# Kernel optimization log

Measured on AMD Instinct MI355X. Metric: run time of the kernel, lower is better.

Reference implementation:

```python
import jax, jax.numpy as jnp
import numpy as np

BIT_DEPTH = 8  # feature squeezing

def setup_inputs() -> dict:
    key = jax.random.key(0)
    ks = jax.random.split(key, 8)
    B, C, H, W = 8, 256, 64, 64
    Cq = C // 8
    x = jax.random.normal(ks[0], (B, C, H, W), dtype=jnp.float32)
    # 1x1 conv weights stored as [out, in] (kernel dims squeezed)
    wq = jax.random.normal(ks[1], (Cq, C), dtype=jnp.float32) * 0.05
    bq = jax.random.normal(ks[2], (Cq,), dtype=jnp.float32) * 0.05
    wk = jax.random.normal(ks[3], (Cq, C), dtype=jnp.float32) * 0.05
    bk = jax.random.normal(ks[4], (Cq,), dtype=jnp.float32) * 0.05
    wv = jax.random.normal(ks[5], (C, C), dtype=jnp.float32) * 0.05
    bv = jax.random.normal(ks[6], (C,), dtype=jnp.float32) * 0.05
    gamma = jax.random.normal(ks[7], (1,), dtype=jnp.float32) * 0.1
    return {"x": x, "wq": wq, "bq": bq, "wk": wk, "bk": bk, "wv": wv, "bv": bv, "gamma": gamma}

def reference(x, wq, bq, wk, bk, wv, bv, gamma):
    B, C, H, W = x.shape
    N = H * W
    xf = x.reshape(B, C, N)  # flatten spatial
    # 1x1 convs == per-pixel linear projections
    q = jnp.einsum('bcn,oc->bon', xf, wq) + bq[None, :, None]   # [B, C/8, N]
    k = jnp.einsum('bcn,oc->bon', xf, wk) + bk[None, :, None]   # [B, C/8, N]
    v = jnp.einsum('bcn,oc->bon', xf, wv) + bv[None, :, None]   # [B, C, N]
    energy = jnp.einsum('bcn,bcm->bnm', q, k)                   # [B, N, N] (no scaling, as in source)
    attn = jax.nn.softmax(energy, axis=-1)
    out = jnp.einsum('bcm,bnm->bcn', v, attn).reshape(B, C, H, W)
    out = gamma[0] * out + out               # gamma-scaled residual of attention output
    scale = jnp.float32(2 ** BIT_DEPTH)
    return jnp.floor(out * scale) / scale    # feature squeezing (bit_depth=8)
```

## Files before the change

### kernel.cpp

```cpp
#include <hip/hip_runtime.h>
#include <math.h>

namespace {
constexpr int BB = 8;
constexpr int CH = 256;
constexpr int CQ = 32;
constexpr int NN = 4096;
}

typedef float f32x4 __attribute__((ext_vector_type(4)));
typedef short bf16x8 __attribute__((ext_vector_type(8)));
typedef unsigned short us8 __attribute__((ext_vector_type(8)));

#define MFMA16(a, b, c) __builtin_amdgcn_mfma_f32_16x16x32_bf16(a, b, c, 0, 0, 0)
#define LOG2E 1.4426950408889634f

__device__ __forceinline__ unsigned short f2bf(float x) {
    unsigned int u = __float_as_uint(x);
    u += 0x7fffu + ((u >> 16) & 1u);
    return (unsigned short)(u >> 16);
}
__device__ __forceinline__ float bf2f(unsigned short h) {
    return __uint_as_float(((unsigned int)h) << 16);
}
__device__ __forceinline__ void gload16(const void* g, void* l) {
    __builtin_amdgcn_global_load_lds(
        (const __attribute__((address_space(1))) unsigned int*)g,
        (__attribute__((address_space(3))) unsigned int*)l, 16, 0, 0);
}

__global__ __launch_bounds__(256) void wsplit_kernel(
    const float* __restrict__ wq, const float* __restrict__ wk,
    const float* __restrict__ wv,
    unsigned short* __restrict__ wh, unsigned short* __restrict__ wl)
{
    int idx = blockIdx.x * 256 + threadIdx.x;
    float v;
    if (idx < 8192)       v = wq[idx];
    else if (idx < 16384) v = wk[idx - 8192];
    else                  v = wv[idx - 16384];
    unsigned short hi = f2bf(v);
    wh[idx] = hi;
    wl[idx] = f2bf(v - bf2f(hi));
}

#define PJ_XL 32768
#define PJ_VE 16384
__global__ __launch_bounds__(256, 2) void proj_kernel(
    const float* __restrict__ x,
    const unsigned short* __restrict__ wh, const unsigned short* __restrict__ wl,
    const float* __restrict__ bq, const float* __restrict__ bk,
    const float* __restrict__ bv,
    unsigned short* __restrict__ qh, unsigned short* __restrict__ ql,
    unsigned short* __restrict__ kh, unsigned short* __restrict__ kl,
    unsigned short* __restrict__ vt)
{
    __shared__ __align__(16) unsigned char smem[65536];
    const int t    = threadIdx.x;
    const int lane = t & 63;
    const int w    = t >> 6;
    const int l16  = lane & 15;
    const int quad = lane >> 4;
    const int b    = blockIdx.x >> 6;
    const int n0   = (blockIdx.x & 63) << 6;

    const float* xB = x + (size_t)b * 256 * NN + n0;
    const int n = lane;

    {
        int cc = w;
        float v[8];
        #pragma unroll
        for (int j = 0; j < 8; ++j)
            v[j] = xB[(size_t)(cc * 8 + j) * NN + n];
        us8 h8, l8;
        #pragma unroll
        for (int j = 0; j < 8; ++j) {
            unsigned short hi = f2bf(v[j]);
            h8[j] = hi;
            l8[j] = f2bf(v[j] - bf2f(hi));
        }
        int off = n * 512 + ((cc ^ (n & 7)) << 4);
        *(us8*)(smem + off) = h8;
        *(us8*)(smem + PJ_XL + off) = l8;
    }
    __syncthreads();

    f32x4 acc[5][4] = {};
    #pragma unroll 1
    for (int kc = 0; kc < 8; ++kc) {
        float vnext[8];
        if (kc < 7) {
            int cc = (kc + 1) * 4 + w;
            #pragma unroll
            for (int j = 0; j < 8; ++j)
                vnext[j] = xB[(size_t)(cc * 8 + j) * NN + n];
        }

        bf16x8 ah[5], al[5];
        #pragma unroll
        for (int i = 0; i < 5; ++i) {
            int och = (w * 5 + i) * 16 + l16;
            ah[i] = *(const bf16x8*)(wh + och * 256 + kc * 32 + quad * 8);
            al[i] = *(const bf16x8*)(wl + och * 256 + kc * 32 + quad * 8);
        }
        #pragma unroll
        for (int nt = 0; nt < 4; ++nt) {
            int roff = (nt * 16 + l16) * 512 + (((kc * 4 + quad) ^ (l16 & 7)) * 16);
            bf16x8 bh = *(const bf16x8*)(smem + roff);
            bf16x8 bl = *(const bf16x8*)(smem + PJ_XL + roff);
            #pragma unroll
            for (int i = 0; i < 5; ++i) {
                acc[i][nt] = MFMA16(ah[i], bh, acc[i][nt]);
                acc[i][nt] = MFMA16(al[i], bh, acc[i][nt]);
                acc[i][nt] = MFMA16(ah[i], bl, acc[i][nt]);
            }
        }

        if (kc < 7) {
            int cc = (kc + 1) * 4 + w;
            us8 h8, l8;
            #pragma unroll
            for (int j = 0; j < 8; ++j) {
                unsigned short hi = f2bf(vnext[j]);
                h8[j] = hi;
                l8[j] = f2bf(vnext[j] - bf2f(hi));
            }
            int off = n * 512 + ((cc ^ (n & 7)) << 4);
            *(us8*)(smem + off) = h8;
            *(us8*)(smem + PJ_XL + off) = l8;
        }
        __syncthreads();
    }

    #pragma unroll
    for (int i = 0; i < 5; ++i) {
        int tile = w * 5 + i;
        if (tile < 4) {
            #pragma unroll
            for (int r = 0; r < 4; ++r) {
                int och = tile * 16 + quad * 4 + r;
                float bias = (och < 32) ? bq[och] : bk[och - 32];
                int arr = (och < 32) ? 0 : 2;
                int oq = och & 31;
                #pragma unroll
                for (int nt = 0; nt < 4; ++nt) {
                    float val = acc[i][nt][r] + bias;
                    if (och < 32) val *= LOG2E;
                    unsigned short hi = f2bf(val);
                    unsigned short lo = f2bf(val - bf2f(hi));
                    *(unsigned short*)(smem + arr * 4096 + (nt * 16 + l16) * 64 + oq * 2) = hi;
                    *(unsigned short*)(smem + (arr + 1) * 4096 + (nt * 16 + l16) * 64 + oq * 2) = lo;
                }
            }
        } else {
            #pragma unroll
            for (int r = 0; r < 4; ++r) {
                int voch = tile * 16 + quad * 4 + r - 64;
                float bias = bv[voch];
                #pragma unroll
                for (int nt = 0; nt < 4; ++nt) {
                    *(unsigned short*)(smem + PJ_VE + voch * 136 + (nt * 16 + l16) * 2)
                        = f2bf(acc[i][nt][r] + bias);
                }
            }
        }
    }
    __syncthreads();

    {
        unsigned short* dsts[4] = { qh, ql, kh, kl };
        int arr = t >> 6, nn = t & 63;
        unsigned short* dst = dsts[arr] + ((size_t)b * NN + n0 + nn) * 32;
        #pragma unroll
        for (int i = 0; i < 4; ++i)
            *(us8*)(dst + i * 8) = *(const us8*)(smem + arr * 4096 + nn * 64 + i * 16);
    }
    #pragma unroll
    for (int p = 0; p < 4; ++p) {
        int voch = p * 64 + (t >> 2), piece = t & 3;
        unsigned short* dst = vt + ((size_t)b * CH + voch) * NN + n0 + piece * 16;
        *(us8*)(dst)     = *(const us8*)(smem + PJ_VE + voch * 136 + piece * 32);
        *(us8*)(dst + 8) = *(const us8*)(smem + PJ_VE + voch * 136 + piece * 32 + 16);
    }
}

#define A_P0 0
#define A_P1 8192
#define A_V0 16384
#define A_V1 49152
#define A_SM 16384

__global__ __launch_bounds__(256, 2) void attn_kernel(
    const unsigned short* __restrict__ qh, const unsigned short* __restrict__ ql,
    const unsigned short* __restrict__ kh, const unsigned short* __restrict__ kl,
    const unsigned short* __restrict__ vt, const float* __restrict__ gptr,
    float* __restrict__ out)
{
    __shared__ __align__(16) unsigned char smem[81920];
    const int t    = threadIdx.x;
    const int lane = t & 63;
    const int w    = t >> 6;
    const int l16  = lane & 15;
    const int quad = lane >> 4;
    const int b    = blockIdx.x & 7;
    const int n0   = (blockIdx.x >> 3) << 6;

    bf16x8 qhA[4], qlA[4];
    #pragma unroll
    for (int qt = 0; qt < 4; ++qt) {
        size_t row = (size_t)b * NN + n0 + qt * 16 + l16;
        qhA[qt] = *(const bf16x8*)(qh + row * 32 + quad * 8);
        qlA[qt] = *(const bf16x8*)(ql + row * 32 + quad * 8);
    }

    const unsigned short* khbase = kh + ((size_t)b * NN + w * 16 + l16) * 32 + quad * 8;
    const unsigned short* klbase = kl + ((size_t)b * NN + w * 16 + l16) * 32 + quad * 8;
    const unsigned char*  vtB    = (const unsigned char*)(vt + (size_t)b * CH * NN);

    const unsigned char* vsrc[8];
    int vlds[8];
    #pragma unroll
    for (int j = 0; j < 8; ++j) {
        int idx = j * 256 + t;
        int r = idx >> 3, cl = idx & 7;
        int cg = cl ^ (r & 7);
        vsrc[j] = vtB + (size_t)r * 8192 + cg * 16;
        vlds[j] = idx * 16;
    }
    const int poff = l16 * 128 + ((((w << 1) | (quad >> 1)) ^ (l16 & 7)) << 4)
                   + ((quad & 1) << 3);

    f32x4 acc[4][4] = {};
    float S[4] = {};

    bf16x8 kch = *(const bf16x8*)(khbase);
    bf16x8 kcl = *(const bf16x8*)(klbase);
    #pragma unroll
    for (int j = 0; j < 8; ++j)
        gload16(vsrc[j], smem + A_V0 + vlds[j]);

    #pragma unroll 1
    for (int tile = 0; tile < 64; ++tile) {
        unsigned char* P = smem + ((tile & 1) ? A_P1 : A_P0);

        f32x4 e4[4];
        __builtin_amdgcn_s_setprio(1);
        #pragma unroll
        for (int qt = 0; qt < 4; ++qt) {
            f32x4 e = { 0.f, 0.f, 0.f, 0.f };
            e = MFMA16(kch, qhA[qt], e);
            e = MFMA16(kch, qlA[qt], e);
            e = MFMA16(kcl, qhA[qt], e);
            e4[qt] = e;
        }
        __builtin_amdgcn_s_setprio(0);

        #pragma unroll
        for (int qt = 0; qt < 4; ++qt) {
            float p0 = exp2f(e4[qt][0]), p1 = exp2f(e4[qt][1]);
            float p2 = exp2f(e4[qt][2]), p3 = exp2f(e4[qt][3]);
            unsigned int u01, u23;
            asm("v_cvt_pk_bf16_f32 %0, %1, %2" : "=v"(u01) : "v"(p0), "v"(p1));
            asm("v_cvt_pk_bf16_f32 %0, %1, %2" : "=v"(u23) : "v"(p2), "v"(p3));
            S[qt] += (__uint_as_float(u01 << 16) + __uint_as_float(u01 & 0xffff0000u))
                   + (__uint_as_float(u23 << 16) + __uint_as_float(u23 & 0xffff0000u));
            int2 pk2 = { (int)u01, (int)u23 };
            *(int2*)(P + qt * 2048 + poff) = pk2;
        }

        __syncthreads();

        const int m1 = ((tile + 1) & 63) * 64;
        bf16x8 knh = *(const bf16x8*)(khbase + (size_t)m1 * 32);
        bf16x8 knl = *(const bf16x8*)(klbase + (size_t)m1 * 32);
        if (tile < 63) {
            unsigned char* vdst = smem + ((tile & 1) ? A_V0 : A_V1);
            #pragma unroll
            for (int j = 0; j < 8; ++j) {
                vsrc[j] += 128;
                gload16(vsrc[j], vdst + vlds[j]);
            }
        }

        const unsigned char* VB = smem + ((tile & 1) ? A_V1 : A_V0);
        bf16x8 af0[4], af1[4], bf0[4], bf1[4];
        #pragma unroll
        for (int qt = 0; qt < 4; ++qt) {
            int row = qt * 16 + l16;
            af0[qt] = *(const bf16x8*)(P + row * 128
                                         + (((0 * 4 + quad) ^ (l16 & 7)) << 4));
            af1[qt] = *(const bf16x8*)(P + row * 128
                                         + (((1 * 4 + quad) ^ (l16 & 7)) << 4));
        }
        #pragma unroll
        for (int ct = 0; ct < 4; ++ct) {
            int vrow = w * 64 + ct * 16 + l16;
            bf0[ct] = *(const bf16x8*)(VB + vrow * 128
                                          + (((0 * 4 + quad) ^ (l16 & 7)) << 4));
            bf1[ct] = *(const bf16x8*)(VB + vrow * 128
                                          + (((1 * 4 + quad) ^ (l16 & 7)) << 4));
        }
        __builtin_amdgcn_s_setprio(1);
        #pragma unroll
        for (int qt = 0; qt < 4; ++qt)
            #pragma unroll
            for (int ct = 0; ct < 4; ++ct)
                acc[qt][ct] = MFMA16(af0[qt], bf0[ct], acc[qt][ct]);
        #pragma unroll
        for (int qt = 0; qt < 4; ++qt)
            #pragma unroll
            for (int ct = 0; ct < 4; ++ct)
                acc[qt][ct] = MFMA16(af1[qt], bf1[ct], acc[qt][ct]);
        __builtin_amdgcn_s_setprio(0);

        kch = knh;
        kcl = knl;
    }

    #pragma unroll
    for (int mask = 16; mask <= 32; mask <<= 1)
        #pragma unroll
        for (int qt = 0; qt < 4; ++qt)
            S[qt] += __shfl_xor(S[qt], mask);
    float* SM = (float*)(smem + A_SM);
    if (quad == 0) {
        #pragma unroll
        for (int qt = 0; qt < 4; ++qt)
            SM[w * 64 + qt * 16 + l16] = S[qt];
    }
    __syncthreads();

    const float g1 = 1.f + gptr[0];
    float* ob = out + (size_t)b * CH * NN;
    #pragma unroll
    for (int qt = 0; qt < 4; ++qt) {
        float is[4];
        #pragma unroll
        for (int r = 0; r < 4; ++r) {
            int qi = qt * 16 + quad * 4 + r;
            float Sf = SM[qi] + SM[64 + qi] + SM[128 + qi] + SM[192 + qi];
            is[r] = g1 / Sf;
        }
        #pragma unroll
        for (int ct = 0; ct < 4; ++ct) {
            float4 o4;
            o4.x = floorf(acc[qt][ct][0] * is[0] * 256.f) * 0.00390625f;
            o4.y = floorf(acc[qt][ct][1] * is[1] * 256.f) * 0.00390625f;
            o4.z = floorf(acc[qt][ct][2] * is[2] * 256.f) * 0.00390625f;
            o4.w = floorf(acc[qt][ct][3] * is[3] * 256.f) * 0.00390625f;
            *(float4*)(ob + (size_t)(w * 64 + ct * 16 + l16) * NN
                          + n0 + qt * 16 + quad * 4) = o4;
        }
    }
}

extern "C" void kernel_launch(void* const* d_in, const int* in_sizes, int n_in,
                              void* d_out, int out_size, void* d_ws, size_t ws_size,
                              hipStream_t stream) {
    const float* x  = (const float*)d_in[0];
    const float* wq = (const float*)d_in[1];
    const float* bq = (const float*)d_in[2];
    const float* wk = (const float*)d_in[3];
    const float* bk = (const float*)d_in[4];
    const float* wv = (const float*)d_in[5];
    const float* bv = (const float*)d_in[6];
    const float* gm = (const float*)d_in[7];
    float* out = (float*)d_out;

    unsigned short* ws = (unsigned short*)d_ws;
    const size_t WSZ = 320 * 256;
    const size_t QSZ = (size_t)BB * NN * 32;
    const size_t XSZ = (size_t)BB * NN * 256;
    unsigned short* wh = ws;
    unsigned short* wl = wh + WSZ;
    unsigned short* qh = wl + WSZ;
    unsigned short* ql = qh + QSZ;
    unsigned short* kh = ql + QSZ;
    unsigned short* kl = kh + QSZ;
    unsigned short* vt = kl + QSZ;

    wsplit_kernel<<<320, 256, 0, stream>>>(wq, wk, wv, wh, wl);
    proj_kernel<<<512, 256, 0, stream>>>(x, wh, wl, bq, bk, bv,
                                         qh, ql, kh, kl, vt);
    attn_kernel<<<512, 256, 0, stream>>>(qh, ql, kh, kl, vt, gm, out);
}
```

Measured before the change: 223.6 us.

## Halve projection tile width to 32 pixels and double block count

The projection kernel now processes 32 spatial positions per block instead of 64. It launches 1024 blocks, uses 32KB of shared memory, and declares launch bounds for 4 blocks per CU. The load schedule becomes 4 stages of 8 channel groups, and the LDS staging and store mapping for Q/K/V are reworked to fit. The goal is more occupancy and parallelism in the projection stage, at the cost of reloading the weight fragments twice as often per pixel. The attention kernel, which likely dominates total time, is unchanged.

```diff
diff --git a/kernel.cpp b/kernel.cpp
--- a/kernel.cpp
+++ b/kernel.cpp
@@ -44,9 +44,7 @@
     wl[idx] = f2bf(v - bf2f(hi));
 }
 
-#define PJ_XL 32768
-#define PJ_VE 16384
-__global__ __launch_bounds__(256, 2) void proj_kernel(
+__global__ __launch_bounds__(256, 4) void proj_kernel(
     const float* __restrict__ x,
     const unsigned short* __restrict__ wh, const unsigned short* __restrict__ wl,
     const float* __restrict__ bq, const float* __restrict__ bk,
@@ -55,20 +53,21 @@
     unsigned short* __restrict__ kh, unsigned short* __restrict__ kl,
     unsigned short* __restrict__ vt)
 {
-    __shared__ __align__(16) unsigned char smem[65536];
+    __shared__ __align__(16) unsigned char smem[32768];
     const int t    = threadIdx.x;
     const int lane = t & 63;
     const int w    = t >> 6;
     const int l16  = lane & 15;
     const int quad = lane >> 4;
-    const int b    = blockIdx.x >> 6;
-    const int n0   = (blockIdx.x & 63) << 6;
+    const int b    = blockIdx.x >> 7;
+    const int n0   = (blockIdx.x & 127) << 5;
 
     const float* xB = x + (size_t)b * 256 * NN + n0;
-    const int n = lane;
+    const int n   = t & 31;
+    const int cg0 = t >> 5;
 
     {
-        int cc = w;
+        int cc = cg0;
         float v[8];
         #pragma unroll
         for (int j = 0; j < 8; ++j)
@@ -82,43 +81,48 @@
         }
         int off = n * 512 + ((cc ^ (n & 7)) << 4);
         *(us8*)(smem + off) = h8;
-        *(us8*)(smem + PJ_XL + off) = l8;
+        *(us8*)(smem + 16384 + off) = l8;
     }
     __syncthreads();
 
-    f32x4 acc[5][4] = {};
+    f32x4 acc[5][2] = {};
     #pragma unroll 1
-    for (int kc = 0; kc < 8; ++kc) {
+    for (int s = 0; s < 4; ++s) {
         float vnext[8];
-        if (kc < 7) {
-            int cc = (kc + 1) * 4 + w;
+        if (s < 3) {
+            int cc = (s + 1) * 8 + cg0;
             #pragma unroll
             for (int j = 0; j < 8; ++j)
                 vnext[j] = xB[(size_t)(cc * 8 + j) * NN + n];
         }
 
-        bf16x8 ah[5], al[5];
-        #pragma unroll
-        for (int i = 0; i < 5; ++i) {
-            int och = (w * 5 + i) * 16 + l16;
-            ah[i] = *(const bf16x8*)(wh + och * 256 + kc * 32 + quad * 8);
-            al[i] = *(const bf16x8*)(wl + och * 256 + kc * 32 + quad * 8);
-        }
-        #pragma unroll
-        for (int nt = 0; nt < 4; ++nt) {
-            int roff = (nt * 16 + l16) * 512 + (((kc * 4 + quad) ^ (l16 & 7)) * 16);
-            bf16x8 bh = *(const bf16x8*)(smem + roff);
-            bf16x8 bl = *(const bf16x8*)(smem + PJ_XL + roff);
+        #pragma unroll
+        for (int kh2 = 0; kh2 < 2; ++kh2) {
+            int kc = s * 2 + kh2;
+            bf16x8 ah[5], al[5];
             #pragma unroll
             for (int i = 0; i < 5; ++i) {
-                acc[i][nt] = MFMA16(ah[i], bh, acc[i][nt]);
-                acc[i][nt] = MFMA16(al[i], bh, acc[i][nt]);
-                acc[i][nt] = MFMA16(ah[i], bl, acc[i][nt]);
-            }
-        }
-
-        if (kc < 7) {
-            int cc = (kc + 1) * 4 + w;
+                int och = (w * 5 + i) * 16 + l16;
+                ah[i] = *(const bf16x8*)(wh + och * 256 + kc * 32 + quad * 8);
+                al[i] = *(const bf16x8*)(wl + och * 256 + kc * 32 + quad * 8);
+            }
+            #pragma unroll
+            for (int nt = 0; nt < 2; ++nt) {
+                int roff = (nt * 16 + l16) * 512
+                         + (((kc * 4 + quad) ^ (l16 & 7)) * 16);
+                bf16x8 bh = *(const bf16x8*)(smem + roff);
+                bf16x8 bl = *(const bf16x8*)(smem + 16384 + roff);
+                #pragma unroll
+                for (int i = 0; i < 5; ++i) {
+                    acc[i][nt] = MFMA16(ah[i], bh, acc[i][nt]);
+                    acc[i][nt] = MFMA16(al[i], bh, acc[i][nt]);
+                    acc[i][nt] = MFMA16(ah[i], bl, acc[i][nt]);
+                }
+            }
+        }
+
+        if (s < 3) {
+            int cc = (s + 1) * 8 + cg0;
             us8 h8, l8;
             #pragma unroll
             for (int j = 0; j < 8; ++j) {
@@ -128,7 +132,7 @@
             }
             int off = n * 512 + ((cc ^ (n & 7)) << 4);
             *(us8*)(smem + off) = h8;
-            *(us8*)(smem + PJ_XL + off) = l8;
+            *(us8*)(smem + 16384 + off) = l8;
         }
         __syncthreads();
     }
@@ -144,13 +148,13 @@
                 int arr = (och < 32) ? 0 : 2;
                 int oq = och & 31;
                 #pragma unroll
-                for (int nt = 0; nt < 4; ++nt) {
+                for (int nt = 0; nt < 2; ++nt) {
                     float val = acc[i][nt][r] + bias;
                     if (och < 32) val *= LOG2E;
                     unsigned short hi = f2bf(val);
                     unsigned short lo = f2bf(val - bf2f(hi));
-                    *(unsigned short*)(smem + arr * 4096 + (nt * 16 + l16) * 64 + oq * 2) = hi;
-                    *(unsigned short*)(smem + (arr + 1) * 4096 + (nt * 16 + l16) * 64 + oq * 2) = lo;
+                    *(unsigned short*)(smem + arr * 2048 + (nt * 16 + l16) * 64 + oq * 2) = hi;
+                    *(unsigned short*)(smem + (arr + 1) * 2048 + (nt * 16 + l16) * 64 + oq * 2) = lo;
                 }
             }
         } else {
@@ -159,8 +163,8 @@
                 int voch = tile * 16 + quad * 4 + r - 64;
                 float bias = bv[voch];
                 #pragma unroll
-                for (int nt = 0; nt < 4; ++nt) {
-                    *(unsigned short*)(smem + PJ_VE + voch * 136 + (nt * 16 + l16) * 2)
+                for (int nt = 0; nt < 2; ++nt) {
+                    *(unsigned short*)(smem + 8192 + voch * 72 + (nt * 16 + l16) * 2)
                         = f2bf(acc[i][nt][r] + bias);
                 }
             }
@@ -170,18 +174,18 @@
 
     {
         unsigned short* dsts[4] = { qh, ql, kh, kl };
-        int arr = t >> 6, nn = t & 63;
-        unsigned short* dst = dsts[arr] + ((size_t)b * NN + n0 + nn) * 32;
+        int arr = t >> 6, sub = t & 63;
+        int row = sub >> 1, half = sub & 1;
+        unsigned short* dst = dsts[arr] + ((size_t)b * NN + n0 + row) * 32 + half * 16;
+        *(us8*)(dst)     = *(const us8*)(smem + arr * 2048 + row * 64 + half * 32);
+        *(us8*)(dst + 8) = *(const us8*)(smem + arr * 2048 + row * 64 + half * 32 + 8 * 2);
+    }
+    {
+        int voch = t;
+        unsigned short* dst = vt + ((size_t)b * CH + voch) * NN + n0;
         #pragma unroll
         for (int i = 0; i < 4; ++i)
-            *(us8*)(dst + i * 8) = *(const us8*)(smem + arr * 4096 + nn * 64 + i * 16);
-    }
-    #pragma unroll
-    for (int p = 0; p < 4; ++p) {
-        int voch = p * 64 + (t >> 2), piece = t & 3;
-        unsigned short* dst = vt + ((size_t)b * CH + voch) * NN + n0 + piece * 16;
-        *(us8*)(dst)     = *(const us8*)(smem + PJ_VE + voch * 136 + piece * 32);
-        *(us8*)(dst + 8) = *(const us8*)(smem + PJ_VE + voch * 136 + piece * 32 + 16);
+            *(us8*)(dst + i * 8) = *(const us8*)(smem + 8192 + voch * 72 + i * 16);
     }
 }
 
@@ -381,7 +385,7 @@
     unsigned short* vt = kl + QSZ;
 
     wsplit_kernel<<<320, 256, 0, stream>>>(wq, wk, wv, wh, wl);
-    proj_kernel<<<512, 256, 0, stream>>>(x, wh, wl, bq, bk, bv,
-                                         qh, ql, kh, kl, vt);
+    proj_kernel<<<1024, 256, 0, stream>>>(x, wh, wl, bq, bk, bv,
+                                          qh, ql, kh, kl, vt);
     attn_kernel<<<512, 256, 0, stream>>>(qh, ql, kh, kl, vt, gm, out);
 }
```

Measured after the change: 265.6 us. +18.8%, slower.

## Split projection output channels across two blocks with double-buffered small LDS

Applied to the files above, without the earlier changes.

The projection kernel now launches twice as many blocks, each handling half the output-channel tiles (12 or 8 tiles), so per-thread accumulators shrink from 5 to 3 tiles. The staged x slice is reduced to a double-buffered 8 KB chunk per k-step instead of holding all 256 channels, cutting LDS from 64 KB to about 33 KB and allowing four blocks per CU. The trade-off is that each x tile is loaded and bf16-split twice, once per half, and the channel split is uneven across the two halves.

```diff
diff --git a/kernel.cpp b/kernel.cpp
--- a/kernel.cpp
+++ b/kernel.cpp
@@ -44,9 +44,7 @@
     wl[idx] = f2bf(v - bf2f(hi));
 }
 
-#define PJ_XL 32768
-#define PJ_VE 16384
-__global__ __launch_bounds__(256, 2) void proj_kernel(
+__global__ __launch_bounds__(256, 4) void proj_kernel(
     const float* __restrict__ x,
     const unsigned short* __restrict__ wh, const unsigned short* __restrict__ wl,
     const float* __restrict__ bq, const float* __restrict__ bk,
@@ -55,24 +53,27 @@
     unsigned short* __restrict__ kh, unsigned short* __restrict__ kl,
     unsigned short* __restrict__ vt)
 {
-    __shared__ __align__(16) unsigned char smem[65536];
+    __shared__ __align__(16) unsigned char smem[33792];
     const int t    = threadIdx.x;
     const int lane = t & 63;
     const int w    = t >> 6;
     const int l16  = lane & 15;
     const int quad = lane >> 4;
-    const int b    = blockIdx.x >> 6;
-    const int n0   = (blockIdx.x & 63) << 6;
+    const int b    = blockIdx.x >> 7;
+    const int h    = blockIdx.x & 1;
+    const int n0   = ((blockIdx.x >> 1) & 63) << 6;
+    const int NT   = h ? 2 : 3;
 
     const float* xB = x + (size_t)b * 256 * NN + n0;
     const int n = lane;
+    const int woff = n * 64 + ((w ^ (n & 3) ^ ((n >> 2) & 3)) << 4);
+    const int rsw  = ((l16 & 3) ^ ((l16 >> 2) & 3));
 
     {
-        int cc = w;
         float v[8];
         #pragma unroll
         for (int j = 0; j < 8; ++j)
-            v[j] = xB[(size_t)(cc * 8 + j) * NN + n];
+            v[j] = xB[(size_t)(w * 8 + j) * NN + n];
         us8 h8, l8;
         #pragma unroll
         for (int j = 0; j < 8; ++j) {
@@ -80,45 +81,49 @@
             h8[j] = hi;
             l8[j] = f2bf(v[j] - bf2f(hi));
         }
-        int off = n * 512 + ((cc ^ (n & 7)) << 4);
-        *(us8*)(smem + off) = h8;
-        *(us8*)(smem + PJ_XL + off) = l8;
+        *(us8*)(smem + woff) = h8;
+        *(us8*)(smem + 4096 + woff) = l8;
     }
     __syncthreads();
 
-    f32x4 acc[5][4] = {};
+    f32x4 acc[3][4] = {};
     #pragma unroll 1
     for (int kc = 0; kc < 8; ++kc) {
         float vnext[8];
         if (kc < 7) {
-            int cc = (kc + 1) * 4 + w;
             #pragma unroll
             for (int j = 0; j < 8; ++j)
-                vnext[j] = xB[(size_t)(cc * 8 + j) * NN + n];
-        }
-
-        bf16x8 ah[5], al[5];
-        #pragma unroll
-        for (int i = 0; i < 5; ++i) {
-            int och = (w * 5 + i) * 16 + l16;
-            ah[i] = *(const bf16x8*)(wh + och * 256 + kc * 32 + quad * 8);
-            al[i] = *(const bf16x8*)(wl + och * 256 + kc * 32 + quad * 8);
+                vnext[j] = xB[(size_t)((kc + 1) * 32 + w * 8 + j) * NN + n];
+        }
+
+        const int base = (kc & 1) * 8192;
+        bf16x8 ah[3], al[3];
+        #pragma unroll
+        for (int i = 0; i < 3; ++i) {
+            if (i < NT) {
+                int tile = h ? (12 + w * 2 + i) : (w * 3 + i);
+                int och  = tile * 16 + l16;
+                ah[i] = *(const bf16x8*)(wh + och * 256 + kc * 32 + quad * 8);
+                al[i] = *(const bf16x8*)(wl + och * 256 + kc * 32 + quad * 8);
+            }
         }
         #pragma unroll
         for (int nt = 0; nt < 4; ++nt) {
-            int roff = (nt * 16 + l16) * 512 + (((kc * 4 + quad) ^ (l16 & 7)) * 16);
-            bf16x8 bh = *(const bf16x8*)(smem + roff);
-            bf16x8 bl = *(const bf16x8*)(smem + PJ_XL + roff);
-            #pragma unroll
-            for (int i = 0; i < 5; ++i) {
-                acc[i][nt] = MFMA16(ah[i], bh, acc[i][nt]);
-                acc[i][nt] = MFMA16(al[i], bh, acc[i][nt]);
-                acc[i][nt] = MFMA16(ah[i], bl, acc[i][nt]);
+            int roff = (nt * 16 + l16) * 64 + ((quad ^ rsw) << 4);
+            bf16x8 bh = *(const bf16x8*)(smem + base + roff);
+            bf16x8 bl = *(const bf16x8*)(smem + base + 4096 + roff);
+            #pragma unroll
+            for (int i = 0; i < 3; ++i) {
+                if (i < NT) {
+                    acc[i][nt] = MFMA16(ah[i], bh, acc[i][nt]);
+                    acc[i][nt] = MFMA16(al[i], bh, acc[i][nt]);
+                    acc[i][nt] = MFMA16(ah[i], bl, acc[i][nt]);
+                }
             }
         }
 
         if (kc < 7) {
-            int cc = (kc + 1) * 4 + w;
+            const int nb = ((kc + 1) & 1) * 8192;
             us8 h8, l8;
             #pragma unroll
             for (int j = 0; j < 8; ++j) {
@@ -126,16 +131,16 @@
                 h8[j] = hi;
                 l8[j] = f2bf(vnext[j] - bf2f(hi));
             }
-            int off = n * 512 + ((cc ^ (n & 7)) << 4);
-            *(us8*)(smem + off) = h8;
-            *(us8*)(smem + PJ_XL + off) = l8;
+            *(us8*)(smem + nb + woff) = h8;
+            *(us8*)(smem + nb + 4096 + woff) = l8;
         }
         __syncthreads();
     }
 
     #pragma unroll
-    for (int i = 0; i < 5; ++i) {
-        int tile = w * 5 + i;
+    for (int i = 0; i < 3; ++i) {
+        if (i >= NT) continue;
+        int tile = h ? (12 + w * 2 + i) : (w * 3 + i);
         if (tile < 4) {
             #pragma unroll
             for (int r = 0; r < 4; ++r) {
@@ -156,11 +161,12 @@
         } else {
             #pragma unroll
             for (int r = 0; r < 4; ++r) {
-                int voch = tile * 16 + quad * 4 + r - 64;
-                float bias = bv[voch];
+                int vloc = tile * 16 + quad * 4 + r - (h ? 192 : 64);
+                float bias = bv[vloc + (h ? 128 : 0)];
+                int vb = h ? 0 : 16384;
                 #pragma unroll
                 for (int nt = 0; nt < 4; ++nt) {
-                    *(unsigned short*)(smem + PJ_VE + voch * 136 + (nt * 16 + l16) * 2)
+                    *(unsigned short*)(smem + vb + vloc * 136 + (nt * 16 + l16) * 2)
                         = f2bf(acc[i][nt][r] + bias);
                 }
             }
@@ -168,20 +174,26 @@
     }
     __syncthreads();
 
-    {
+    if (h == 0) {
         unsigned short* dsts[4] = { qh, ql, kh, kl };
-        int arr = t >> 6, nn = t & 63;
-        unsigned short* dst = dsts[arr] + ((size_t)b * NN + n0 + nn) * 32;
+        int arr = t >> 6, nn2 = t & 63;
+        unsigned short* dst = dsts[arr] + ((size_t)b * NN + n0 + nn2) * 32;
         #pragma unroll
         for (int i = 0; i < 4; ++i)
-            *(us8*)(dst + i * 8) = *(const us8*)(smem + arr * 4096 + nn * 64 + i * 16);
-    }
-    #pragma unroll
-    for (int p = 0; p < 4; ++p) {
-        int voch = p * 64 + (t >> 2), piece = t & 3;
-        unsigned short* dst = vt + ((size_t)b * CH + voch) * NN + n0 + piece * 16;
-        *(us8*)(dst)     = *(const us8*)(smem + PJ_VE + voch * 136 + piece * 32);
-        *(us8*)(dst + 8) = *(const us8*)(smem + PJ_VE + voch * 136 + piece * 32 + 16);
+            *(us8*)(dst + i * 8) = *(const us8*)(smem + arr * 4096 + nn2 * 64 + i * 16);
+        int voch = t >> 1, piece = t & 1;
+        unsigned short* vd = vt + ((size_t)b * CH + voch) * NN + n0 + piece * 32;
+        const unsigned char* src = smem + 16384 + voch * 136 + piece * 64;
+        #pragma unroll
+        for (int i = 0; i < 4; ++i)
+            *(us8*)(vd + i * 8) = *(const us8*)(src + i * 16);
+    } else {
+        int vloc = t >> 1, piece = t & 1;
+        unsigned short* vd = vt + ((size_t)b * CH + vloc + 128) * NN + n0 + piece * 32;
+        const unsigned char* src = smem + vloc * 136 + piece * 64;
+        #pragma unroll
+        for (int i = 0; i < 4; ++i)
+            *(us8*)(vd + i * 8) = *(const us8*)(src + i * 16);
     }
 }
 
@@ -381,7 +393,7 @@
     unsigned short* vt = kl + QSZ;
 
     wsplit_kernel<<<320, 256, 0, stream>>>(wq, wk, wv, wh, wl);
-    proj_kernel<<<512, 256, 0, stream>>>(x, wh, wl, bq, bk, bv,
-                                         qh, ql, kh, kl, vt);
+    proj_kernel<<<1024, 256, 0, stream>>>(x, wh, wl, bq, bk, bv,
+                                          qh, ql, kh, kl, vt);
     attn_kernel<<<512, 256, 0, stream>>>(qh, ql, kh, kl, vt, gm, out);
 }
```

New measurement: 236.0 us. +5.6%, slower.
